# Optimization experiments

Measured on AMD Instinct MI355X. Metric: run time of the kernel, lower is better.

## Reference

```python
import jax, jax.numpy as jnp
import numpy as np

B, T, IN, H, L = 8192, 200, 4, 16, 4
MLP_IN, MLP_HID, MLP_OUT = H * T, 64, IN * 7


def _lstm_layer(x, Wih, Whh, b):
    """x: [B,T,Din]; Wih: [4H,Din]; Whh: [4H,H]; b: [4H]. Returns [B,T,H].
    PyTorch gate order: i, f, g, o."""
    xg = jnp.einsum('btd,gd->btg', x, Wih) + b  # precompute input projections [B,T,4H]
    h0 = jnp.zeros((x.shape[0], H), x.dtype)
    c0 = jnp.zeros((x.shape[0], H), x.dtype)

    def step(carry, xt):
        h, c = carry
        gates = xt + h @ Whh.T  # [B,4H]
        i, f, g, o = jnp.split(gates, 4, axis=-1)
        i = jax.nn.sigmoid(i); f = jax.nn.sigmoid(f)
        g = jnp.tanh(g); o = jax.nn.sigmoid(o)
        c = f * c + i * g
        h = o * jnp.tanh(c)
        return (h, c), h

    _, hs = jax.lax.scan(step, (h0, c0), jnp.swapaxes(xg, 0, 1))  # [T,B,H]
    return jnp.swapaxes(hs, 0, 1)


def setup_inputs() -> dict:
    key = jax.random.key(0)
    ks = jax.random.split(key, 12)
    s = 1.0 / np.sqrt(H)
    u = lambda k, shp: jax.random.uniform(k, shp, jnp.float32, -s, s)
    x = jax.random.normal(ks[0], (B, T, IN), jnp.float32)
    Wih0 = u(ks[1], (4 * H, IN))            # layer 0 input weights
    Wih_rest = u(ks[2], (L - 1, 4 * H, H))  # layers 1..3
    Whh = u(ks[3], (L, 4 * H, H))
    bih = u(ks[4], (L, 4 * H))
    bhh = u(ks[5], (L, 4 * H))
    sm = 1.0 / np.sqrt(MLP_IN)
    W1 = jax.random.uniform(ks[6], (MLP_HID, MLP_IN), jnp.float32, -sm, sm)
    b1 = jax.random.uniform(ks[7], (MLP_HID,), jnp.float32, -sm, sm)
    sm2 = 1.0 / np.sqrt(MLP_HID)
    W2 = jax.random.uniform(ks[8], (MLP_OUT, MLP_HID), jnp.float32, -sm2, sm2)
    b2 = jax.random.uniform(ks[9], (MLP_OUT,), jnp.float32, -sm2, sm2)
    return {"x": x, "Wih0": Wih0, "Wih_rest": Wih_rest, "Whh": Whh,
            "bih": bih, "bhh": bhh, "W1": W1, "b1": b1, "W2": W2, "b2": b2}


def reference(x, Wih0, Wih_rest, Whh, bih, bhh, W1, b1, W2, b2):
    h = _lstm_layer(x, Wih0, Whh[0], bih[0] + bhh[0])
    for l in range(1, L):
        h = _lstm_layer(h, Wih_rest[l - 1], Whh[l], bih[l] + bhh[l])
    flat = h.reshape(-1, H * T)  # [B, 3200]
    hid = jax.nn.relu(flat @ W1.T + b1)
    return hid @ W2.T + b2  # [B, 28]
```

## Files before the change

kernel.cpp:

```cpp
#include <hip/hip_runtime.h>
#include <hip/hip_bf16.h>


typedef short  bf16x8 __attribute__((ext_vector_type(8)));
typedef float  f32x4  __attribute__((ext_vector_type(4)));
typedef unsigned int uint2v __attribute__((ext_vector_type(2)));

namespace {
constexpr int kT    = 200;
constexpr int kOut  = 28;
constexpr int kQ    = kT / 4;
constexpr int kSteps = kQ + 4;
constexpr float kNLog2e  = -1.4426950408889634f;
constexpr float kN2Log2e = -2.8853900817779268f;
constexpr int kW1Elems = 64 * 3200;
constexpr int kRow  = 40;
constexpr int kSlot = 16 * kRow;
constexpr int kLay  = 4 * kSlot;
constexpr int kPar  = 4 * kLay;
}

union FragU { bf16x8 v; unsigned u[4]; };

__device__ __forceinline__ float fast_rcp(float v){ return __builtin_amdgcn_rcpf(v); }
__device__ __forceinline__ float fast_exp2(float v){ return __builtin_amdgcn_exp2f(v); }
__device__ __forceinline__ float sig_scaled(float p){ return fast_rcp(1.0f + fast_exp2(p)); }
__device__ __forceinline__ float tanh_true(float v){
  return fmaf(fast_rcp(1.0f + fast_exp2(kN2Log2e*v)), 2.0f, -1.0f);
}

__device__ __forceinline__ void split8(const float* v, FragU& hi, FragU& lo){
#pragma unroll
  for (int r=0;r<4;++r){
    unsigned ua=__float_as_uint(v[2*r]), ub=__float_as_uint(v[2*r+1]);
    hi.u[r] = (ua>>16) | (ub & 0xffff0000u);
    float af=__uint_as_float(ua & 0xffff0000u);
    float bf=__uint_as_float(ub & 0xffff0000u);
    float al=v[2*r]-af, bl=v[2*r+1]-bf;
    lo.u[r] = (__float_as_uint(al)>>16) | (__float_as_uint(bl) & 0xffff0000u);
  }
}

__global__ __launch_bounds__(256)
void presplit_w1(const float* __restrict__ W1,
                 short* __restrict__ W1h, short* __restrict__ W1l){
  int i = blockIdx.x*256 + threadIdx.x;
  if (i < kW1Elems){
    float v = W1[i];
    unsigned u = __float_as_uint(v);
    float hif = __uint_as_float(u & 0xffff0000u);
    float lo  = v - hif;
    W1h[i] = (short)(u >> 16);
    W1l[i] = (short)(__float_as_uint(lo) >> 16);
  }
}

template<bool PS>
__global__ __launch_bounds__(256)
void lstm_pipe(const float* __restrict__ x,
               const float* __restrict__ Wih0,
               const float* __restrict__ Wihr,
               const float* __restrict__ Whh,
               const float* __restrict__ bih,
               const float* __restrict__ bhh,
               const float* __restrict__ W1,
               const float* __restrict__ b1,
               const float* __restrict__ W2,
               const float* __restrict__ b2,
               const short* __restrict__ W1h,
               const short* __restrict__ W1l,
               float* __restrict__ out)
{
  __shared__ unsigned short H[2*kPar];
  __shared__ float ldsR[16][68];

  const int tid  = threadIdx.x;
  const int lane = tid & 63;
  const int wv   = tid >> 6;
  const int s    = lane & 15;
  const int q    = lane >> 4;
  const int l    = wv;
  const int lm1  = (l==0) ? 0 : (l-1);
  const int sbase = blockIdx.x * 16;

  for (int i = tid; i < 2*kPar/2; i += 256) ((unsigned*)H)[i] = 0u;

  FragU A[4][2];
#pragma unroll
  for (int tile=0;tile<4;++tile){
    const int grow = tile*16 + s;
    const float kE = (tile==2)? kN2Log2e : kNLog2e;
    float v[8];
    if (l==0){
#pragma unroll
      for (int e=0;e<8;++e){
        float w = 0.f;
        if (q==0 && e<4) w = Wih0[grow*4+e];
        if (q>=2)        w = Whh[grow*16 + (q&1)*8 + e];
        v[e] = w*kE;
      }
    } else {
#pragma unroll
      for (int e=0;e<8;++e){
        float w = (q<2) ? Wihr[((l-1)*64+grow)*16 + q*8 + e]
                        : Whh [(( l )*64+grow)*16 + (q&1)*8 + e];
        v[e] = w*kE;
      }
    }
    split8(v, A[tile][0], A[tile][1]);
  }

  f32x4 biasf[4];
#pragma unroll
  for (int tile=0;tile<4;++tile){
    const float kE = (tile==2)? kN2Log2e : kNLog2e;
#pragma unroll
    for (int r=0;r<4;++r){
      const int row = l*64 + tile*16 + 4*q + r;
      biasf[tile][r] = (bih[row] + bhh[row]) * kE;
    }
  }

  float cst[4] = {0.f,0.f,0.f,0.f};
  f32x4 mlpacc = (f32x4){0.f,0.f,0.f,0.f};

  const float* xp = x + (size_t)(sbase+s)*(kT*4);
  float4 xc0,xc1,xc2,xc3;
  if (l==0){
    xc0 = *(const float4*)(xp+ 0); xc1 = *(const float4*)(xp+ 4);
    xc2 = *(const float4*)(xp+ 8); xc3 = *(const float4*)(xp+12);
  }

  const int rowW1 = wv*16 + s;
  const short* w1hp = W1h + (size_t)rowW1*3200;
  const short* w1lp = W1l + (size_t)rowW1*3200;
  const float* w1fp = W1  + (size_t)rowW1*3200;

  const int laneRd = s*kRow + (q&1)*8;
  const int laneWr = s*kRow + q*4;
  auto OFF = [](int par,int layer,int slot){ return par*kPar + layer*kLay + slot*kSlot; };
  const unsigned short* ra0_0 = H + laneRd + ((q<2) ? OFF(1,lm1,0) : OFF(1,l,3));
  const unsigned short* raS_0 = H + laneRd + ((q<2) ? OFF(1,lm1,1) : OFF(0,l,0));
  unsigned short*       wrt_0 = H + laneWr + OFF(0,l,0);
  const unsigned short* mrd_0 = H + laneRd + OFF(1,3,0) + (q>>1)*kSlot;
  const unsigned short* ra0_1 = H + laneRd + ((q<2) ? OFF(0,lm1,0) : OFF(0,l,3));
  const unsigned short* raS_1 = H + laneRd + ((q<2) ? OFF(0,lm1,1) : OFF(1,l,0));
  unsigned short*       wrt_1 = H + laneWr + OFF(1,l,0);
  const unsigned short* mrd_1 = H + laneRd + OFF(0,3,0) + (q>>1)*kSlot;

  __syncthreads();

  auto super = [&](int n, const unsigned short* ra0, const unsigned short* raS,
                   unsigned short* wa, const unsigned short* ma){
    const int m = n - 4;
    FragU WAh0,WAl0,WAh1,WAl1;
    float4 wfa0,wfb0,wfa1,wfb1;
    if (m >= 0 && m < kQ){
      const int off = 64*m + q*8;
      if (PS){
        WAh0.v = *(const bf16x8*)(w1hp + off);
        WAl0.v = *(const bf16x8*)(w1lp + off);
        WAh1.v = *(const bf16x8*)(w1hp + off + 32);
        WAl1.v = *(const bf16x8*)(w1lp + off + 32);
      } else {
        wfa0 = *(const float4*)(w1fp + off);
        wfb0 = *(const float4*)(w1fp + off + 4);
        wfa1 = *(const float4*)(w1fp + off + 32);
        wfb1 = *(const float4*)(w1fp + off + 36);
      }
    }
    const int pr = n - l;
    float4 xn0,xn1,xn2,xn3;
    if (l==0 && pr+1 < kQ){
      const float* xq = xp + 16*(pr+1);
      xn0 = *(const float4*)(xq+ 0); xn1 = *(const float4*)(xq+ 4);
      xn2 = *(const float4*)(xq+ 8); xn3 = *(const float4*)(xq+12);
    }

    if (pr >= 0 && pr < kQ){
#pragma unroll
      for (int st=0; st<4; ++st){
        const unsigned short* rp_ = (st==0) ? ra0 : (raS + (st-1)*kSlot);
        FragU Bh, Bl;
        Bh.v = *(const bf16x8*)(rp_);
        Bl.v = *(const bf16x8*)(rp_ + 16);
        if (l==0){
          const float4 xv = (st==0)?xc0:(st==1)?xc1:(st==2)?xc2:xc3;
          if (q==0){
            const unsigned u0=__float_as_uint(xv.x), u1=__float_as_uint(xv.y);
            const unsigned u2=__float_as_uint(xv.z), u3=__float_as_uint(xv.w);
            Bh.u[0] = (u0>>16)|(u1&0xffff0000u);
            Bh.u[1] = (u2>>16)|(u3&0xffff0000u);
            Bh.u[2] = 0u; Bh.u[3] = 0u;
            const float f0 = xv.x-__uint_as_float(u0&0xffff0000u);
            const float f1 = xv.y-__uint_as_float(u1&0xffff0000u);
            const float f2 = xv.z-__uint_as_float(u2&0xffff0000u);
            const float f3 = xv.w-__uint_as_float(u3&0xffff0000u);
            Bl.u[0] = (__float_as_uint(f0)>>16)|(__float_as_uint(f1)&0xffff0000u);
            Bl.u[1] = (__float_as_uint(f2)>>16)|(__float_as_uint(f3)&0xffff0000u);
            Bl.u[2] = 0u; Bl.u[3] = 0u;
          } else if (q==1){
#pragma unroll
            for (int r=0;r<4;++r){ Bh.u[r]=0u; Bl.u[r]=0u; }
          }
        }

        float si[4], sf[4], sg[4], so[4];
#pragma unroll
        for (int tile=0;tile<4;++tile){
          f32x4 acc = biasf[tile];
          acc = __builtin_amdgcn_mfma_f32_16x16x32_bf16(A[tile][0].v,Bh.v,acc,0,0,0);
          acc = __builtin_amdgcn_mfma_f32_16x16x32_bf16(A[tile][0].v,Bl.v,acc,0,0,0);
          acc = __builtin_amdgcn_mfma_f32_16x16x32_bf16(A[tile][1].v,Bh.v,acc,0,0,0);
#pragma unroll
          for (int r=0;r<4;++r){
            const float a = sig_scaled(acc[r]);
            if      (tile==0) si[r]=a;
            else if (tile==1) sf[r]=a;
            else if (tile==2) sg[r]=fmaf(a,2.f,-1.f);
            else              so[r]=a;
          }
        }
        float hn[4];
#pragma unroll
        for (int r=0;r<4;++r){
          cst[r] = fmaf(sf[r], cst[r], si[r]*sg[r]);
          hn[r] = so[r]*tanh_true(cst[r]);
        }
        {
          const unsigned u0=__float_as_uint(hn[0]), u1=__float_as_uint(hn[1]);
          const unsigned u2=__float_as_uint(hn[2]), u3=__float_as_uint(hn[3]);
          const unsigned hi01 = (u0>>16)|(u1&0xffff0000u);
          const unsigned hi23 = (u2>>16)|(u3&0xffff0000u);
          const float f0 = hn[0]-__uint_as_float(u0&0xffff0000u);
          const float f1 = hn[1]-__uint_as_float(u1&0xffff0000u);
          const float f2 = hn[2]-__uint_as_float(u2&0xffff0000u);
          const float f3 = hn[3]-__uint_as_float(u3&0xffff0000u);
          const unsigned lo01 = (__float_as_uint(f0)>>16)|(__float_as_uint(f1)&0xffff0000u);
          const unsigned lo23 = (__float_as_uint(f2)>>16)|(__float_as_uint(f3)&0xffff0000u);
          *(uint2v*)(wa + st*kSlot)      = (uint2v){hi01,hi23};
          *(uint2v*)(wa + st*kSlot + 16) = (uint2v){lo01,lo23};
        }
      }
    }
    if (l==0 && pr+1 < kQ){ xc0=xn0; xc1=xn1; xc2=xn2; xc3=xn3; }

    if (m >= 0 && m < kQ){
#pragma unroll
      for (int pp=0; pp<2; ++pp){
        const unsigned short* bp = ma + pp*(2*kSlot);
        FragU Bh, Bl;
        Bh.v = *(const bf16x8*)(bp);
        Bl.v = *(const bf16x8*)(bp + 16);
        FragU Ah, Al;
        if (PS){
          Ah = pp ? WAh1 : WAh0;
          Al = pp ? WAl1 : WAl0;
        } else {
          const float4 wa4 = pp ? wfa1 : wfa0;
          const float4 wb4 = pp ? wfb1 : wfb0;
          float v[8] = {wa4.x,wa4.y,wa4.z,wa4.w,wb4.x,wb4.y,wb4.z,wb4.w};
          split8(v,Ah,Al);
        }
        mlpacc = __builtin_amdgcn_mfma_f32_16x16x32_bf16(Ah.v,Bh.v,mlpacc,0,0,0);
        mlpacc = __builtin_amdgcn_mfma_f32_16x16x32_bf16(Ah.v,Bl.v,mlpacc,0,0,0);
        mlpacc = __builtin_amdgcn_mfma_f32_16x16x32_bf16(Al.v,Bh.v,mlpacc,0,0,0);
      }
    }
    __syncthreads();
  };

#pragma unroll 1
  for (int n2 = 0; n2 < kSteps/2; ++n2){
    super(2*n2,   ra0_0, raS_0, wrt_0, mrd_0);
    super(2*n2+1, ra0_1, raS_1, wrt_1, mrd_1);
  }

  {
    f32x4 rv;
#pragma unroll
    for (int r=0;r<4;++r)
      rv[r] = fmaxf(mlpacc[r] + b1[wv*16 + 4*q + r], 0.f);
    *(f32x4*)&ldsR[s][wv*16 + 4*q] = rv;
  }
  __syncthreads();
  {
    const int o  = lane & 31;
    const int oc = (o < kOut) ? o : 0;
    float4 w2r[16];
#pragma unroll
    for (int c2=0;c2<16;++c2) w2r[c2] = *(const float4*)(W2 + oc*64 + 4*c2);
    const float bias2 = b2[oc];
#pragma unroll
    for (int mm=0;mm<2;++mm){
      const int s2 = wv*4 + 2*mm + (lane>>5);
      float a0=bias2, a1=0.f, a2=0.f, a3=0.f;
#pragma unroll
      for (int c2=0;c2<16;++c2){
        const float4 rvv = *(const float4*)&ldsR[s2][4*c2];
        a0 = fmaf(w2r[c2].x, rvv.x, a0);
        a1 = fmaf(w2r[c2].y, rvv.y, a1);
        a2 = fmaf(w2r[c2].z, rvv.z, a2);
        a3 = fmaf(w2r[c2].w, rvv.w, a3);
      }
      if (o < kOut) out[(size_t)(sbase+s2)*kOut + o] = (a0+a1)+(a2+a3);
    }
  }
}

extern "C" void kernel_launch(void* const* d_in, const int* in_sizes, int n_in,
                              void* d_out, int out_size, void* d_ws, size_t ws_size,
                              hipStream_t stream) {
  (void)in_sizes; (void)n_in; (void)out_size;
  const float* x    = (const float*)d_in[0];
  const float* Wih0 = (const float*)d_in[1];
  const float* Wihr = (const float*)d_in[2];
  const float* Whh  = (const float*)d_in[3];
  const float* bih  = (const float*)d_in[4];
  const float* bhh  = (const float*)d_in[5];
  const float* W1   = (const float*)d_in[6];
  const float* b1   = (const float*)d_in[7];
  const float* W2   = (const float*)d_in[8];
  const float* b2   = (const float*)d_in[9];
  float* out = (float*)d_out;

  const size_t splitBytes = (size_t)kW1Elems * sizeof(short) * 2;
  dim3 grid(8192/16), block(256);
  if (ws_size >= splitBytes) {
    short* W1h = (short*)d_ws;
    short* W1l = W1h + kW1Elems;
    hipLaunchKernelGGL(presplit_w1, dim3((kW1Elems+255)/256), dim3(256), 0, stream,
                       W1, W1h, W1l);
    hipLaunchKernelGGL(lstm_pipe<true>, grid, block, 0, stream,
                       x, Wih0, Wihr, Whh, bih, bhh, W1, b1, W2, b2, W1h, W1l, out);
  } else {
    hipLaunchKernelGGL(lstm_pipe<false>, grid, block, 0, stream,
                       x, Wih0, Wihr, Whh, bih, bhh, W1, b1, W2, b2,
                       (const short*)nullptr, (const short*)nullptr, out);
  }
}
```

Before: 266.1 us.

## Presplit x into bf16 hi/lo and merge LSTM gate reciprocals

Adds a prepass kernel that splits the input x into bf16 hi/lo halves in workspace, so layer-0 waves load ready-made fragments instead of splitting floats in the recurrent loop. It also rewrites the gate math to share reciprocals: it computes 1+exp2 denominators for all gates and combines i*g and o*tanh(c) into single rcp calls, clamping c before the tanh exponent. This cuts transcendental and VALU work on the serial critical path. In exchange it adds an extra kernel launch and about 13 MB of extra HBM traffic for the x split, and it needs a larger workspace. If the workspace is too small it falls back to the old split path, which still uses the new gate math.

```diff
diff --git a/kernel.cpp b/kernel.cpp
--- a/kernel.cpp
+++ b/kernel.cpp
@@ -14,6 +14,7 @@
 constexpr float kNLog2e  = -1.4426950408889634f;
 constexpr float kN2Log2e = -2.8853900817779268f;
 constexpr int kW1Elems = 64 * 3200;
+constexpr int kXElems  = 8192 * 200 * 4;
 constexpr int kRow  = 40;
 constexpr int kSlot = 16 * kRow;
 constexpr int kLay  = 4 * kSlot;
@@ -24,10 +25,6 @@
 
 __device__ __forceinline__ float fast_rcp(float v){ return __builtin_amdgcn_rcpf(v); }
 __device__ __forceinline__ float fast_exp2(float v){ return __builtin_amdgcn_exp2f(v); }
-__device__ __forceinline__ float sig_scaled(float p){ return fast_rcp(1.0f + fast_exp2(p)); }
-__device__ __forceinline__ float tanh_true(float v){
-  return fmaf(fast_rcp(1.0f + fast_exp2(kN2Log2e*v)), 2.0f, -1.0f);
-}
 
 __device__ __forceinline__ void split8(const float* v, FragU& hi, FragU& lo){
 #pragma unroll
@@ -42,16 +39,16 @@
 }
 
 __global__ __launch_bounds__(256)
-void presplit_w1(const float* __restrict__ W1,
-                 short* __restrict__ W1h, short* __restrict__ W1l){
+void presplit_pair(const float* __restrict__ src, int n,
+                   short* __restrict__ dh, short* __restrict__ dl){
   int i = blockIdx.x*256 + threadIdx.x;
-  if (i < kW1Elems){
-    float v = W1[i];
+  if (i < n){
+    float v = src[i];
     unsigned u = __float_as_uint(v);
     float hif = __uint_as_float(u & 0xffff0000u);
     float lo  = v - hif;
-    W1h[i] = (short)(u >> 16);
-    W1l[i] = (short)(__float_as_uint(lo) >> 16);
+    dh[i] = (short)(u >> 16);
+    dl[i] = (short)(__float_as_uint(lo) >> 16);
   }
 }
 
@@ -69,6 +66,8 @@
                const float* __restrict__ b2,
                const short* __restrict__ W1h,
                const short* __restrict__ W1l,
+               const short* __restrict__ Xh,
+               const short* __restrict__ Xl,
                float* __restrict__ out)
 {
   __shared__ unsigned short H[2*kPar];
@@ -124,11 +123,22 @@
   float cst[4] = {0.f,0.f,0.f,0.f};
   f32x4 mlpacc = (f32x4){0.f,0.f,0.f,0.f};
 
-  const float* xp = x + (size_t)(sbase+s)*(kT*4);
+  const float* xp  = x  + (size_t)(sbase+s)*(kT*4);
+  const short* xhp = PS ? (Xh + (size_t)(sbase+s)*(kT*4)) : nullptr;
+  const short* xlp = PS ? (Xl + (size_t)(sbase+s)*(kT*4)) : nullptr;
+  uint2v xh_[4], xl_[4];
   float4 xc0,xc1,xc2,xc3;
   if (l==0){
-    xc0 = *(const float4*)(xp+ 0); xc1 = *(const float4*)(xp+ 4);
-    xc2 = *(const float4*)(xp+ 8); xc3 = *(const float4*)(xp+12);
+    if (PS){
+#pragma unroll
+      for (int st=0;st<4;++st){
+        xh_[st] = *(const uint2v*)(xhp + st*4);
+        xl_[st] = *(const uint2v*)(xlp + st*4);
+      }
+    } else {
+      xc0 = *(const float4*)(xp+ 0); xc1 = *(const float4*)(xp+ 4);
+      xc2 = *(const float4*)(xp+ 8); xc3 = *(const float4*)(xp+12);
+    }
   }
 
   const int rowW1 = wv*16 + s;
@@ -170,11 +180,20 @@
       }
     }
     const int pr = n - l;
+    uint2v xhn[4], xln[4];
     float4 xn0,xn1,xn2,xn3;
     if (l==0 && pr+1 < kQ){
-      const float* xq = xp + 16*(pr+1);
-      xn0 = *(const float4*)(xq+ 0); xn1 = *(const float4*)(xq+ 4);
-      xn2 = *(const float4*)(xq+ 8); xn3 = *(const float4*)(xq+12);
+      if (PS){
+#pragma unroll
+        for (int st=0;st<4;++st){
+          xhn[st] = *(const uint2v*)(xhp + 16*(pr+1) + st*4);
+          xln[st] = *(const uint2v*)(xlp + 16*(pr+1) + st*4);
+        }
+      } else {
+        const float* xq = xp + 16*(pr+1);
+        xn0 = *(const float4*)(xq+ 0); xn1 = *(const float4*)(xq+ 4);
+        xn2 = *(const float4*)(xq+ 8); xn3 = *(const float4*)(xq+12);
+      }
     }
 
     if (pr >= 0 && pr < kQ){
@@ -185,27 +204,32 @@
         Bh.v = *(const bf16x8*)(rp_);
         Bl.v = *(const bf16x8*)(rp_ + 16);
         if (l==0){
-          const float4 xv = (st==0)?xc0:(st==1)?xc1:(st==2)?xc2:xc3;
           if (q==0){
-            const unsigned u0=__float_as_uint(xv.x), u1=__float_as_uint(xv.y);
-            const unsigned u2=__float_as_uint(xv.z), u3=__float_as_uint(xv.w);
-            Bh.u[0] = (u0>>16)|(u1&0xffff0000u);
-            Bh.u[1] = (u2>>16)|(u3&0xffff0000u);
-            Bh.u[2] = 0u; Bh.u[3] = 0u;
-            const float f0 = xv.x-__uint_as_float(u0&0xffff0000u);
-            const float f1 = xv.y-__uint_as_float(u1&0xffff0000u);
-            const float f2 = xv.z-__uint_as_float(u2&0xffff0000u);
-            const float f3 = xv.w-__uint_as_float(u3&0xffff0000u);
-            Bl.u[0] = (__float_as_uint(f0)>>16)|(__float_as_uint(f1)&0xffff0000u);
-            Bl.u[1] = (__float_as_uint(f2)>>16)|(__float_as_uint(f3)&0xffff0000u);
-            Bl.u[2] = 0u; Bl.u[3] = 0u;
+            if (PS){
+              Bh.u[0]=xh_[st][0]; Bh.u[1]=xh_[st][1]; Bh.u[2]=0u; Bh.u[3]=0u;
+              Bl.u[0]=xl_[st][0]; Bl.u[1]=xl_[st][1]; Bl.u[2]=0u; Bl.u[3]=0u;
+            } else {
+              const float4 xv = (st==0)?xc0:(st==1)?xc1:(st==2)?xc2:xc3;
+              const unsigned u0=__float_as_uint(xv.x), u1=__float_as_uint(xv.y);
+              const unsigned u2=__float_as_uint(xv.z), u3=__float_as_uint(xv.w);
+              Bh.u[0] = (u0>>16)|(u1&0xffff0000u);
+              Bh.u[1] = (u2>>16)|(u3&0xffff0000u);
+              Bh.u[2] = 0u; Bh.u[3] = 0u;
+              const float f0 = xv.x-__uint_as_float(u0&0xffff0000u);
+              const float f1 = xv.y-__uint_as_float(u1&0xffff0000u);
+              const float f2 = xv.z-__uint_as_float(u2&0xffff0000u);
+              const float f3 = xv.w-__uint_as_float(u3&0xffff0000u);
+              Bl.u[0] = (__float_as_uint(f0)>>16)|(__float_as_uint(f1)&0xffff0000u);
+              Bl.u[1] = (__float_as_uint(f2)>>16)|(__float_as_uint(f3)&0xffff0000u);
+              Bl.u[2] = 0u; Bl.u[3] = 0u;
+            }
           } else if (q==1){
 #pragma unroll
             for (int r=0;r<4;++r){ Bh.u[r]=0u; Bl.u[r]=0u; }
           }
         }
 
-        float si[4], sf[4], sg[4], so[4];
+        float Dt[4][4];
 #pragma unroll
         for (int tile=0;tile<4;++tile){
           f32x4 acc = biasf[tile];
@@ -213,19 +237,21 @@
           acc = __builtin_amdgcn_mfma_f32_16x16x32_bf16(A[tile][0].v,Bl.v,acc,0,0,0);
           acc = __builtin_amdgcn_mfma_f32_16x16x32_bf16(A[tile][1].v,Bh.v,acc,0,0,0);
 #pragma unroll
-          for (int r=0;r<4;++r){
-            const float a = sig_scaled(acc[r]);
-            if      (tile==0) si[r]=a;
-            else if (tile==1) sf[r]=a;
-            else if (tile==2) sg[r]=fmaf(a,2.f,-1.f);
-            else              so[r]=a;
-          }
+          for (int r=0;r<4;++r) Dt[tile][r] = 1.0f + fast_exp2(acc[r]);
         }
         float hn[4];
 #pragma unroll
         for (int r=0;r<4;++r){
-          cst[r] = fmaf(sf[r], cst[r], si[r]*sg[r]);
-          hn[r] = so[r]*tanh_true(cst[r]);
+          const float Rf  = fast_rcp(Dt[1][r]);
+          const float Rig = fast_rcp(Dt[0][r]*Dt[2][r]);
+          const float ig  = (2.0f - Dt[2][r])*Rig;
+          float cn = fmaf(cst[r], Rf, ig);
+          cst[r] = cn;
+          cn = fminf(fmaxf(cn, -10.0f), 10.0f);
+          const float Ec = fast_exp2(kN2Log2e*cn);
+          const float Dc = 1.0f + Ec;
+          const float Roc = fast_rcp(Dt[3][r]*Dc);
+          hn[r] = (2.0f - Dc)*Roc;
         }
         {
           const unsigned u0=__float_as_uint(hn[0]), u1=__float_as_uint(hn[1]);
@@ -243,7 +269,12 @@
         }
       }
     }
-    if (l==0 && pr+1 < kQ){ xc0=xn0; xc1=xn1; xc2=xn2; xc3=xn3; }
+    if (l==0 && pr+1 < kQ){
+      if (PS){
+#pragma unroll
+        for (int st=0;st<4;++st){ xh_[st]=xhn[st]; xl_[st]=xln[st]; }
+      } else { xc0=xn0; xc1=xn1; xc2=xn2; xc3=xn3; }
+    }
 
     if (m >= 0 && m < kQ){
 #pragma unroll
@@ -324,18 +355,24 @@
   const float* b2   = (const float*)d_in[9];
   float* out = (float*)d_out;
 
-  const size_t splitBytes = (size_t)kW1Elems * sizeof(short) * 2;
+  const size_t needBytes = ((size_t)kW1Elems*2 + (size_t)kXElems*2) * sizeof(short);
   dim3 grid(8192/16), block(256);
-  if (ws_size >= splitBytes) {
+  if (ws_size >= needBytes) {
     short* W1h = (short*)d_ws;
     short* W1l = W1h + kW1Elems;
-    hipLaunchKernelGGL(presplit_w1, dim3((kW1Elems+255)/256), dim3(256), 0, stream,
-                       W1, W1h, W1l);
+    short* Xh  = W1l + kW1Elems;
+    short* Xl  = Xh + kXElems;
+    hipLaunchKernelGGL(presplit_pair, dim3((kW1Elems+255)/256), dim3(256), 0, stream,
+                       W1, kW1Elems, W1h, W1l);
+    hipLaunchKernelGGL(presplit_pair, dim3((kXElems+255)/256), dim3(256), 0, stream,
+                       x, kXElems, Xh, Xl);
     hipLaunchKernelGGL(lstm_pipe<true>, grid, block, 0, stream,
-                       x, Wih0, Wihr, Whh, bih, bhh, W1, b1, W2, b2, W1h, W1l, out);
+                       x, Wih0, Wihr, Whh, bih, bhh, W1, b1, W2, b2,
+                       W1h, W1l, Xh, Xl, out);
   } else {
     hipLaunchKernelGGL(lstm_pipe<false>, grid, block, 0, stream,
                        x, Wih0, Wihr, Whh, bih, bhh, W1, b1, W2, b2,
+                       (const short*)nullptr, (const short*)nullptr,
                        (const short*)nullptr, (const short*)nullptr, out);
   }
 }
```

Result: slower. 275.1 us (+3.4%).
